# Kernel tuning notes

Measured on AMD Instinct MI355X. Metric: run time of the kernel, lower is better.

Reference implementation:

```python
import jax, jax.numpy as jnp
import numpy as np

N = 20000      # nodes
E = 320000     # edges (avg degree 16)
F_IN = 512     # post_features
H1, H2 = 1024, 512   # hard-coded GCN hidden widths
F_OUT = 128    # post_embedding
D1, D2 = 152, 48     # hard-coded Dense widths


def setup_inputs() -> dict:
    key = jax.random.key(0)
    ks = jax.random.split(key, 16)
    inp = {
        "x": jax.random.normal(ks[0], (N, F_IN), dtype=jnp.float32),
        "src": jax.random.randint(ks[1], (E,), 0, N, dtype=jnp.int32),
        "dst": jax.random.randint(ks[2], (E,), 0, N, dtype=jnp.int32),
        "edge_weight": jax.random.uniform(ks[3], (E,), dtype=jnp.float32) / 16.0,
        # GCN layer params (xavier-ish scale)
        "W1": jax.random.normal(ks[4], (F_IN, H1), dtype=jnp.float32) * (2.0 / (F_IN + H1)) ** 0.5,
        "b1": jax.random.uniform(ks[5], (H1,), dtype=jnp.float32),
        "W2": jax.random.normal(ks[6], (H1, H2), dtype=jnp.float32) * (2.0 / (H1 + H2)) ** 0.5,
        "b2": jax.random.uniform(ks[7], (H2,), dtype=jnp.float32),
        "W3": jax.random.normal(ks[8], (H2, F_OUT), dtype=jnp.float32) * (2.0 / (H2 + F_OUT)) ** 0.5,
        "b3": jax.random.uniform(ks[9], (F_OUT,), dtype=jnp.float32),
        # Dense head params
        "Wd1": jax.random.normal(ks[10], (F_OUT, D1), dtype=jnp.float32) * (2.0 / F_OUT) ** 0.5,
        "bd1": jnp.zeros((D1,), dtype=jnp.float32),
        "Wd2": jax.random.normal(ks[11], (D1, D2), dtype=jnp.float32) * (2.0 / D1) ** 0.5,
        "bd2": jnp.zeros((D2,), dtype=jnp.float32),
        "Wd3": jax.random.normal(ks[12], (D2, 1), dtype=jnp.float32) * (2.0 / D2) ** 0.5,
        "bd3": jnp.zeros((1,), dtype=jnp.float32),
    }
    return inp


def _spmm(src, dst, w, h, n):
    # out[i] = sum_{e: dst[e]==i} w[e] * h[src[e]]  == A @ h with A sparse COO
    return jax.ops.segment_sum(w[:, None] * h[src], dst, num_segments=n)


def reference(x, src, dst, edge_weight, W1, b1, W2, b2, W3, b3,
              Wd1, bd1, Wd2, bd2, Wd3, bd3):
    n = x.shape[0]
    # GCN layer: x @ W -> spmm(A, .) -> + bias ; tanh between layers 1,2
    h = jnp.tanh(_spmm(src, dst, edge_weight, x @ W1, n) + b1)
    h = jnp.tanh(_spmm(src, dst, edge_weight, h @ W2, n) + b2)
    g = _spmm(src, dst, edge_weight, h @ W3, n) + b3
    # F.dropout treated as identity (deterministic reference / eval mode)
    d = jax.nn.relu(g @ Wd1 + bd1)
    d = jax.nn.relu(d @ Wd2 + bd2)
    d = d @ Wd3 + bd3
    return d
```

## Files before the change

### kernel.cpp

```cpp
#include <hip/hip_runtime.h>
#include <hip/hip_bf16.h>


typedef __attribute__((ext_vector_type(8))) short bf16x8;
typedef __attribute__((ext_vector_type(8))) unsigned short u16x8;
typedef __attribute__((ext_vector_type(4))) float f32x4;
typedef unsigned short u16;

#define MPAD 20096
#define AS1 __attribute__((address_space(1)))
#define AS3 __attribute__((address_space(3)))

__device__ inline u16 f2b(float f) {
  union { float f; unsigned int u; } x; x.f = f;
  unsigned int r = x.u + 0x7FFFu + ((x.u >> 16) & 1u);
  return (u16)(r >> 16);
}
__device__ inline float b2f(u16 u) {
  union { unsigned int u; float f; } x; x.u = ((unsigned int)u) << 16; return x.f;
}
__device__ inline unsigned int cvt_pk_bf16(float lo, float hi) {
  unsigned int r;
  asm("v_cvt_pk_bf16_f32 %0, %1, %2" : "=v"(r) : "v"(lo), "v"(hi));
  return r;
}
__device__ inline float fast_tanh(float x) {
  float cx = fminf(fmaxf(x, -9.f), 9.f);
  float e = __expf(2.f * cx);
  float d = e + 1.f, r;
  asm("v_rcp_f32 %0, %1" : "=v"(r) : "v"(d));
  return (e - 1.f) * r;
}


__device__ inline void wT_tile(const float* __restrict__ W, u16* __restrict__ WT,
                               int K, int N, int KPAD, int NPAD,
                               int bx, int by, float (*tile)[33]) {
  const int kb = by * 32, nb = bx * 32;
  const int tx = threadIdx.x & 31, ty = threadIdx.x >> 5;
  #pragma unroll
  for (int i = 0; i < 4; ++i) {
    int k = kb + ty + i * 8, n = nb + tx;
    tile[ty + i * 8][tx] = (k < K && n < N) ? W[(size_t)k * N + n] : 0.f;
  }
  __syncthreads();
  #pragma unroll
  for (int i = 0; i < 4; ++i) {
    int n = nb + ty + i * 8, k = kb + tx;
    WT[(size_t)n * KPAD + k] = f2b(tile[tx][ty + i * 8]);
  }
}

__global__ __launch_bounds__(256) void prep_all(
    const float* __restrict__ x, u16* __restrict__ xb,
    const float* __restrict__ W1, u16* __restrict__ w1t,
    const float* __restrict__ W2, u16* __restrict__ w2t,
    const float* __restrict__ W3, u16* __restrict__ w3t,
    const float* __restrict__ Wd1, u16* __restrict__ wd1t,
    const float* __restrict__ Wd2, u16* __restrict__ wd2t,
    const float* __restrict__ bd1, float* __restrict__ bd1p,
    const float* __restrict__ bd2, float* __restrict__ bd2p,
    const int* __restrict__ dst, int* __restrict__ cnt1,
    int* __restrict__ cnt2) {
  __shared__ float tile[32][33];
  const int b = blockIdx.x;
  const int tid = threadIdx.x;
  if (b < 512) {
    wT_tile(W1, w1t, 512, 1024, 512, 1024, b % 32, b / 32, tile);
  } else if (b < 1024) {
    int t = b - 512;  wT_tile(W2, w2t, 1024, 512, 1024, 512, t % 16, t / 16, tile);
  } else if (b < 1088) {
    int t = b - 1024; wT_tile(W3, w3t, 512, 128, 512, 128, t % 4, t / 4, tile);
  } else if (b < 1120) {
    int t = b - 1088; wT_tile(Wd1, wd1t, 128, 152, 128, 256, t % 8, t / 8, tile);
  } else if (b < 1152) {
    int t = b - 1120; wT_tile(Wd2, wd2t, 152, 48, 256, 128, t % 4, t / 4, tile);
  } else if (b < 11152) {
    int idx = ((b - 1152) * 256 + tid) * 4;
    if (idx < 20000 * 512) {
      float4 v = *reinterpret_cast<const float4*>(&x[idx]);
      uint2 o;
      o.x = cvt_pk_bf16(v.x, v.y);
      o.y = cvt_pk_bf16(v.z, v.w);
      *reinterpret_cast<uint2*>(&xb[idx]) = o;
    }
  } else if (b == 11152) {
    bd1p[tid] = (tid < 152) ? bd1[tid] : 0.f;
  } else if (b == 11153) {
    if (tid < 128) bd2p[tid] = (tid < 48) ? bd2[tid] : 0.f;
  } else if (b < 12404) {
    int e = (b - 11154) * 256 + tid;
    if (e < 320000) atomicAdd(&cnt1[dst[e]], 1);
  } else {
    int i = (b - 12404) * 256 + tid;
    if (i < 20000) cnt2[i] = 0;
  }
}

__global__ __launch_bounds__(1024) void scan_part(
    const int* __restrict__ in, int* __restrict__ out,
    int* __restrict__ bsum, int n) {
  __shared__ int wsum[16];
  const int lane = threadIdx.x & 63, wv = threadIdx.x >> 6;
  int i = blockIdx.x * 1024 + threadIdx.x;
  int v = (i < n) ? in[i] : 0;
  int s = v;
  #pragma unroll
  for (int off = 1; off < 64; off <<= 1) {
    int t = __shfl_up(s, off, 64);
    if (lane >= off) s += t;
  }
  if (lane == 63) wsum[wv] = s;
  __syncthreads();
  if (wv == 0 && lane < 16) {
    int t = wsum[lane];
    #pragma unroll
    for (int off = 1; off < 16; off <<= 1) {
      int u = __shfl_up(t, off, 64);
      if (lane >= off) t += u;
    }
    wsum[lane] = t;
  }
  __syncthreads();
  int waveoff = (wv == 0) ? 0 : wsum[wv - 1];
  if (i < n) out[i] = waveoff + s - v;
  if (threadIdx.x == 0) bsum[blockIdx.x] = wsum[15];
}
__global__ __launch_bounds__(1024) void scan_fix(
    int* __restrict__ out, const int* __restrict__ bsum, int n, int nb) {
  int b = blockIdx.x;
  int pre = 0, tot = 0;
  for (int j = 0; j < nb; ++j) {
    int v = bsum[j];
    if (j < b) pre += v;
    tot += v;
  }
  int i = b * 1024 + threadIdx.x;
  if (i < n && b > 0) out[i] += pre;
  if (b == 0 && threadIdx.x == 0) out[n] = tot;
}

__global__ __launch_bounds__(256) void scatter_csr(
    const int* __restrict__ dst, const int* __restrict__ src,
    const float* __restrict__ ew, const int* __restrict__ row_ptr,
    int* __restrict__ cnt, int* __restrict__ csr_src,
    float* __restrict__ csr_w, int E) {
  int e = blockIdx.x * 256 + threadIdx.x;
  if (e >= E) return;
  int d = dst[e];
  int pos = row_ptr[d] + atomicAdd(&cnt[d], 1);
  csr_src[pos] = src[e];
  csr_w[pos] = ew[e];
}

template <int ACT, bool BIAS, bool OUT_BF16>
__global__ __launch_bounds__(256) void gemm_mfma_db(
    const u16* __restrict__ A, const u16* __restrict__ BT,
    const float* __restrict__ bias, void* __restrict__ C,
    int M, int K, int Nn) {
  __shared__ __align__(16) u16 As[2][128 * 64];
  __shared__ __align__(16) u16 Bs[2][128 * 64];
  const int tid = threadIdx.x;
  const int lane = tid & 63;
  const int wave = tid >> 6;
  const int lo = lane & 15, hi = lane >> 4;
  const int wr = wave >> 1, wc = wave & 1;

  const int gx = gridDim.x;
  const int nwg = gx * gridDim.y;
  const int wg = blockIdx.y * gx + blockIdx.x;
  const int q = nwg >> 3, r = nwg & 7;
  const int xcd = wg & 7, sidx = wg >> 3;
  const int swz = (xcd < r ? xcd * (q + 1) : r * (q + 1) + (xcd - r) * q) + sidx;
  const int row0 = (swz / gx) * 128;
  const int col0 = (swz % gx) * 128;

  const u16* pa[4];
  const u16* pb[4];
  int so[4];
  #pragma unroll
  for (int i = 0; i < 4; ++i) {
    int o = i * 4096 + tid * 16;
    int rr = o >> 7;
    int ke = ((o & 127) >> 1) ^ ((rr & 7) << 3);
    pa[i] = &A[(size_t)(row0 + rr) * K + ke];
    pb[i] = &BT[(size_t)(col0 + rr) * K + ke];
    so[i] = o >> 1;
  }

  const int nk = K >> 6;
  f32x4 acc[4][4] = {};

  auto STAGE = [&](int buf, int kt) {
    const int ko = kt << 6;
    #pragma unroll
    for (int i = 0; i < 4; ++i) {
      __builtin_amdgcn_global_load_lds(
          (const AS1 void*)(pa[i] + ko),
          (AS3 void*)&As[buf][so[i]], 16, 0, 0);
      __builtin_amdgcn_global_load_lds(
          (const AS1 void*)(pb[i] + ko),
          (AS3 void*)&Bs[buf][so[i]], 16, 0, 0);
    }
  };

  STAGE(0, 0);
  STAGE(1, 1);
  asm volatile("s_waitcnt vmcnt(8)" ::: "memory");
  __builtin_amdgcn_s_barrier();

  auto body = [&](int cur, int kt) {
    bf16x8 af[2][4], bfr[2][4];
    #pragma unroll
    for (int ks = 0; ks < 2; ++ks) {
      #pragma unroll
      for (int m = 0; m < 4; ++m) {
        int row = wr * 64 + m * 16 + lo;
        int idx = (row * 64 + ks * 32 + hi * 8) ^ ((row & 7) << 3);
        af[ks][m] = *reinterpret_cast<const bf16x8*>(&As[cur][idx]);
      }
      #pragma unroll
      for (int n = 0; n < 4; ++n) {
        int col = wc * 64 + n * 16 + lo;
        int idx = (col * 64 + ks * 32 + hi * 8) ^ ((col & 7) << 3);
        bfr[ks][n] = *reinterpret_cast<const bf16x8*>(&Bs[cur][idx]);
      }
    }
    __builtin_amdgcn_s_setprio(1);
    #pragma unroll
    for (int ks = 0; ks < 2; ++ks)
      #pragma unroll
      for (int m = 0; m < 4; ++m)
        #pragma unroll
        for (int n = 0; n < 4; ++n)
          acc[m][n] = __builtin_amdgcn_mfma_f32_16x16x32_bf16(
              af[ks][m], bfr[ks][n], acc[m][n], 0, 0, 0);
    __builtin_amdgcn_s_setprio(0);
    asm volatile("s_waitcnt lgkmcnt(0)" ::: "memory");
    __builtin_amdgcn_s_barrier();
    if (kt + 2 < nk) {
      STAGE(cur, kt + 2);
      asm volatile("s_waitcnt vmcnt(8)" ::: "memory");
    } else if (kt + 1 < nk) {
      asm volatile("s_waitcnt vmcnt(0)" ::: "memory");
    }
    __builtin_amdgcn_s_barrier();
  };

  for (int kt = 0; kt < nk; kt += 2) {
    body(0, kt);
    body(1, kt + 1);
  }

  float bv[4];
  if (BIAS) {
    #pragma unroll
    for (int n = 0; n < 4; ++n) bv[n] = bias[col0 + wc * 64 + n * 16 + lo];
  }

  u16* Cb = (u16*)C;
  float* Cf = (float*)C;
  #pragma unroll
  for (int m = 0; m < 4; ++m) {
    int rbase = row0 + wr * 64 + m * 16 + hi * 4;
    #pragma unroll
    for (int n = 0; n < 4; ++n) {
      int c = col0 + wc * 64 + n * 16 + lo;
      float vv[4];
      #pragma unroll
      for (int i = 0; i < 4; ++i) {
        float v = acc[m][n][i];
        if (BIAS) v += bv[n];
        if (ACT == 1) v = fast_tanh(v);
        else if (ACT == 2) v = fmaxf(v, 0.f);
        vv[i] = v;
      }
      if (OUT_BF16) {
        unsigned int r01 = cvt_pk_bf16(vv[0], vv[1]);
        unsigned int r23 = cvt_pk_bf16(vv[2], vv[3]);
        u16* p = Cb + (size_t)rbase * Nn + c;
        p[0]              = (u16)r01;
        p[Nn]             = (u16)(r01 >> 16);
        p[2 * (size_t)Nn] = (u16)r23;
        p[3 * (size_t)Nn] = (u16)(r23 >> 16);
      } else {
        float* p = Cf + (size_t)rbase * Nn + c;
        p[0] = vv[0]; p[Nn] = vv[1];
        p[2 * (size_t)Nn] = vv[2]; p[3 * (size_t)Nn] = vv[3];
      }
    }
  }
}

template <int ACT, bool BIAS, bool OUT_BF16>
__global__ __launch_bounds__(256) void spmm_wave512(
    const int* __restrict__ row_ptr, const int* __restrict__ csr_src,
    const float* __restrict__ csr_w, const u16* __restrict__ H,
    const float* __restrict__ bias, void* __restrict__ out, int N) {
  __shared__ int s_src[4][64];
  __shared__ float s_w[4][64];
  const int wv = threadIdx.x >> 6;
  const int lane = threadIdx.x & 63;
  const int node = blockIdx.x * 4 + wv;
  if (node >= N) return;
  const int c = lane * 8;
  const int beg = row_ptr[node], end = row_ptr[node + 1];

  float a[8] = {};
  for (int p = beg; p < end; p += 64) {
    int cnt = end - p;
    if (cnt > 64) cnt = 64;
    if (lane < cnt) {
      s_src[wv][lane] = csr_src[p + lane];
      s_w[wv][lane] = csr_w[p + lane];
    }
    asm volatile("s_waitcnt lgkmcnt(0)" ::: "memory");
    int j = 0;
    for (; j + 7 < cnt; j += 8) {
      int ss[8]; float ww[8]; u16x8 hh[8];
      #pragma unroll
      for (int u = 0; u < 8; ++u) { ss[u] = s_src[wv][j + u]; ww[u] = s_w[wv][j + u]; }
      #pragma unroll
      for (int u = 0; u < 8; ++u)
        hh[u] = *reinterpret_cast<const u16x8*>(&H[(size_t)ss[u] * 512 + c]);
      #pragma unroll
      for (int u = 0; u < 8; ++u)
        #pragma unroll
        for (int k = 0; k < 8; ++k) a[k] += ww[u] * b2f(hh[u][k]);
    }
    for (; j < cnt; ++j) {
      int s = s_src[wv][j];
      float wt = s_w[wv][j];
      u16x8 hv = *reinterpret_cast<const u16x8*>(&H[(size_t)s * 512 + c]);
      #pragma unroll
      for (int k = 0; k < 8; ++k) a[k] += wt * b2f(hv[k]);
    }
    asm volatile("s_waitcnt lgkmcnt(0)" ::: "memory");
  }
  if (BIAS) {
    #pragma unroll
    for (int k = 0; k < 8; ++k) a[k] += bias[c + k];
  }
  if (ACT == 1) {
    #pragma unroll
    for (int k = 0; k < 8; ++k) a[k] = fast_tanh(a[k]);
  }
  if (OUT_BF16) {
    uint4 o;
    o.x = cvt_pk_bf16(a[0], a[1]);
    o.y = cvt_pk_bf16(a[2], a[3]);
    o.z = cvt_pk_bf16(a[4], a[5]);
    o.w = cvt_pk_bf16(a[6], a[7]);
    *reinterpret_cast<uint4*>(&((u16*)out)[(size_t)node * 512 + c]) = o;
  } else {
    float* op = &((float*)out)[(size_t)node * 512 + c];
    #pragma unroll
    for (int k = 0; k < 8; ++k) op[k] = a[k];
  }
}

template <int F, int ACT, bool BIAS, bool OUT_BF16>
__global__ __launch_bounds__(256) void spmm_small(
    const int* __restrict__ row_ptr, const int* __restrict__ csr_src,
    const float* __restrict__ csr_w, const u16* __restrict__ H,
    const float* __restrict__ bias, void* __restrict__ out, int N) {
  constexpr int TPN = F / 8;
  constexpr int NPB = 256 / TPN;
  int sub = threadIdx.x / TPN;
  int ln = threadIdx.x - sub * TPN;
  int node = blockIdx.x * NPB + sub;
  if (node >= N) return;
  int c = ln * 8;
  int beg = row_ptr[node], end = row_ptr[node + 1];
  float a[8] = {};
  int p = beg;
  for (; p + 3 < end; p += 4) {
    int s0 = csr_src[p], s1 = csr_src[p + 1], s2 = csr_src[p + 2], s3 = csr_src[p + 3];
    float w0 = csr_w[p], w1 = csr_w[p + 1], w2 = csr_w[p + 2], w3 = csr_w[p + 3];
    u16x8 h0 = *reinterpret_cast<const u16x8*>(&H[(size_t)s0 * F + c]);
    u16x8 h1 = *reinterpret_cast<const u16x8*>(&H[(size_t)s1 * F + c]);
    u16x8 h2 = *reinterpret_cast<const u16x8*>(&H[(size_t)s2 * F + c]);
    u16x8 h3 = *reinterpret_cast<const u16x8*>(&H[(size_t)s3 * F + c]);
    #pragma unroll
    for (int k = 0; k < 8; ++k)
      a[k] += w0 * b2f(h0[k]) + w1 * b2f(h1[k]) +
              w2 * b2f(h2[k]) + w3 * b2f(h3[k]);
  }
  for (; p < end; ++p) {
    int s = csr_src[p];
    float wt = csr_w[p];
    u16x8 hv = *reinterpret_cast<const u16x8*>(&H[(size_t)s * F + c]);
    #pragma unroll
    for (int k = 0; k < 8; ++k) a[k] += wt * b2f(hv[k]);
  }
  if (BIAS) {
    #pragma unroll
    for (int k = 0; k < 8; ++k) a[k] += bias[c + k];
  }
  if (ACT == 1) {
    #pragma unroll
    for (int k = 0; k < 8; ++k) a[k] = fast_tanh(a[k]);
  }
  if (OUT_BF16) {
    uint4 o;
    o.x = cvt_pk_bf16(a[0], a[1]);
    o.y = cvt_pk_bf16(a[2], a[3]);
    o.z = cvt_pk_bf16(a[4], a[5]);
    o.w = cvt_pk_bf16(a[6], a[7]);
    *reinterpret_cast<uint4*>(&((u16*)out)[(size_t)node * F + c]) = o;
  } else {
    float* op = &((float*)out)[(size_t)node * F + c];
    #pragma unroll
    for (int k = 0; k < 8; ++k) op[k] = a[k];
  }
}

__global__ __launch_bounds__(256) void last_layer_bf16(
    const u16* __restrict__ D2v, const float* __restrict__ W,
    const float* __restrict__ b, float* __restrict__ out,
    int M, int K, int ld) {
  int rr = blockIdx.x * 256 + threadIdx.x;
  if (rr >= M) return;
  float s = b[0];
  const u16* row = &D2v[(size_t)rr * ld];
  #pragma unroll 8
  for (int k = 0; k < 48; ++k) s += b2f(row[k]) * W[k];
  out[rr] = s;
}


extern "C" void kernel_launch(void* const* d_in, const int* in_sizes, int n_in,
                              void* d_out, int out_size, void* d_ws, size_t ws_size,
                              hipStream_t stream) {
  const int N = 20000, E = 320000;
  const int F_IN = 512, H1 = 1024, H2 = 512, F_OUT = 128;
  const int D1P = 256, D2P = 128;

  const float* x    = (const float*)d_in[0];
  const int*   src  = (const int*)d_in[1];
  const int*   dst  = (const int*)d_in[2];
  const float* ew   = (const float*)d_in[3];
  const float* W1   = (const float*)d_in[4];
  const float* b1   = (const float*)d_in[5];
  const float* W2   = (const float*)d_in[6];
  const float* b2   = (const float*)d_in[7];
  const float* W3   = (const float*)d_in[8];
  const float* b3   = (const float*)d_in[9];
  const float* Wd1  = (const float*)d_in[10];
  const float* bd1  = (const float*)d_in[11];
  const float* Wd2  = (const float*)d_in[12];
  const float* bd2  = (const float*)d_in[13];
  const float* Wd3  = (const float*)d_in[14];
  const float* bd3  = (const float*)d_in[15];
  float* out = (float*)d_out;

  size_t off = 0;
  auto alloc = [&](size_t bytes) {
    void* p = (char*)d_ws + off;
    off += (bytes + 255) & ~(size_t)255;
    return p;
  };
  u16* xb   = (u16*)alloc((size_t)MPAD * F_IN * 2);
  u16* ax   = (u16*)alloc((size_t)MPAD * F_IN * 2);
  u16* h1   = (u16*)alloc((size_t)MPAD * H1 * 2);
  u16* w1t  = (u16*)alloc((size_t)H1 * F_IN * 2);
  u16* w2t  = (u16*)alloc((size_t)H2 * H1 * 2);
  u16* w3t  = (u16*)alloc((size_t)F_OUT * H2 * 2);
  u16* wd1t = (u16*)alloc((size_t)D1P * F_OUT * 2);
  u16* wd2t = (u16*)alloc((size_t)D2P * D1P * 2);
  float* bd1p = (float*)alloc((size_t)D1P * 4);
  float* bd2p = (float*)alloc((size_t)D2P * 4);
  int* row_ptr = (int*)alloc((size_t)(N + 1) * 4);
  int* cnt1    = (int*)alloc((size_t)N * 4);
  int* cnt2    = (int*)alloc((size_t)N * 4);
  int* bsum    = (int*)alloc((size_t)32 * 4);
  int* csr_src = (int*)alloc((size_t)E * 4);
  float* csr_w = (float*)alloc((size_t)E * 4);

  u16* t2 = xb;
  u16* h2 = ax;
  u16* t3 = h1;
  u16* gb = t3 + (size_t)MPAD * F_OUT;
  u16* d1 = gb + (size_t)MPAD * F_OUT;
  u16* d2 = d1 + (size_t)MPAD * D1P;

  auto cdiv = [](int a, int b) { return (a + b - 1) / b; };

  hipMemsetAsync(cnt1, 0, (size_t)N * 4, stream);
  prep_all<<<12483, 256, 0, stream>>>(x, xb, W1, w1t, W2, w2t, W3, w3t,
                                      Wd1, wd1t, Wd2, wd2t, bd1, bd1p,
                                      bd2, bd2p, dst, cnt1, cnt2);
  scan_part<<<20, 1024, 0, stream>>>(cnt1, row_ptr, bsum, N);
  scan_fix<<<20, 1024, 0, stream>>>(row_ptr, bsum, N, 20);
  scatter_csr<<<cdiv(E, 256), 256, 0, stream>>>(dst, src, ew, row_ptr, cnt2,
                                                csr_src, csr_w, E);

  spmm_wave512<0, false, true><<<cdiv(N, 4), 256, 0, stream>>>(
      row_ptr, csr_src, csr_w, xb, nullptr, ax, N);
  gemm_mfma_db<1, true, true><<<dim3(H1 / 128, MPAD / 128), 256, 0, stream>>>(
      ax, w1t, b1, h1, MPAD, F_IN, H1);

  gemm_mfma_db<0, false, true><<<dim3(H2 / 128, MPAD / 128), 256, 0, stream>>>(
      h1, w2t, nullptr, t2, MPAD, H1, H2);
  spmm_wave512<1, true, true><<<cdiv(N, 4), 256, 0, stream>>>(
      row_ptr, csr_src, csr_w, t2, b2, h2, N);

  gemm_mfma_db<0, false, true><<<dim3(F_OUT / 128, MPAD / 128), 256, 0, stream>>>(
      h2, w3t, nullptr, t3, MPAD, H2, F_OUT);
  spmm_small<128, 0, true, true><<<cdiv(N, 16), 256, 0, stream>>>(
      row_ptr, csr_src, csr_w, t3, b3, gb, N);

  gemm_mfma_db<2, true, true><<<dim3(D1P / 128, MPAD / 128), 256, 0, stream>>>(
      gb, wd1t, bd1p, d1, MPAD, F_OUT, D1P);
  gemm_mfma_db<2, true, true><<<dim3(D2P / 128, MPAD / 128), 256, 0, stream>>>(
      d1, wd2t, bd2p, d2, MPAD, D1P, D2P);
  last_layer_bf16<<<cdiv(N, 256), 256, 0, stream>>>(d2, Wd3, bd3, out, N, 48, D2P);
}
```

Measured before the change: 252.0 us.

## Pack CSR src/weight into u32 and split SpMM columns into per-XCD chunks

Packs each edge's source index (16 bits) and bf16-rounded weight into one 32-bit word, which halves CSR index traffic. The SpMM kernels are replaced by one kernel that splits the feature columns into chunks, with consecutive block IDs handling the same nodes' different column chunks. The intent is that the chunks land on different XCDs, so each XCD's L2 holds only a slice of H and cache locality improves. It depends on N < 65536 and on round-robin XCD dispatch, and it rounds edge weights to bf16, which costs some precision.

```diff
diff --git a/kernel.cpp b/kernel.cpp
--- a/kernel.cpp
+++ b/kernel.cpp
@@ -143,14 +143,12 @@
 __global__ __launch_bounds__(256) void scatter_csr(
     const int* __restrict__ dst, const int* __restrict__ src,
     const float* __restrict__ ew, const int* __restrict__ row_ptr,
-    int* __restrict__ cnt, int* __restrict__ csr_src,
-    float* __restrict__ csr_w, int E) {
+    int* __restrict__ cnt, unsigned int* __restrict__ csr_pack, int E) {
   int e = blockIdx.x * 256 + threadIdx.x;
   if (e >= E) return;
   int d = dst[e];
   int pos = row_ptr[d] + atomicAdd(&cnt[d], 1);
-  csr_src[pos] = src[e];
-  csr_w[pos] = ew[e];
+  csr_pack[pos] = ((unsigned int)f2b(ew[e]) << 16) | (unsigned int)src[e];
 }
 
 template <int ACT, bool BIAS, bool OUT_BF16>
@@ -292,126 +290,57 @@
   }
 }
 
-template <int ACT, bool BIAS, bool OUT_BF16>
-__global__ __launch_bounds__(256) void spmm_wave512(
-    const int* __restrict__ row_ptr, const int* __restrict__ csr_src,
-    const float* __restrict__ csr_w, const u16* __restrict__ H,
-    const float* __restrict__ bias, void* __restrict__ out, int N) {
-  __shared__ int s_src[4][64];
-  __shared__ float s_w[4][64];
-  const int wv = threadIdx.x >> 6;
-  const int lane = threadIdx.x & 63;
-  const int node = blockIdx.x * 4 + wv;
+template <int F, int CHUNKS, int ACT, bool BIAS, bool OUT_BF16>
+__global__ __launch_bounds__(256) void spmm_xcd(
+    const int* __restrict__ row_ptr, const unsigned int* __restrict__ pack,
+    const u16* __restrict__ H, const float* __restrict__ bias,
+    void* __restrict__ out, int N) {
+  const int ci = blockIdx.x % CHUNKS;
+  const int nb = blockIdx.x / CHUNKS;
+  const int g = threadIdx.x >> 4;
+  const int gl = threadIdx.x & 15;
+  const int node = nb * 16 + g;
   if (node >= N) return;
-  const int c = lane * 8;
+  const int c0 = ci * (F / CHUNKS) + gl * 4;
   const int beg = row_ptr[node], end = row_ptr[node + 1];
 
-  float a[8] = {};
-  for (int p = beg; p < end; p += 64) {
-    int cnt = end - p;
-    if (cnt > 64) cnt = 64;
-    if (lane < cnt) {
-      s_src[wv][lane] = csr_src[p + lane];
-      s_w[wv][lane] = csr_w[p + lane];
-    }
-    asm volatile("s_waitcnt lgkmcnt(0)" ::: "memory");
-    int j = 0;
-    for (; j + 7 < cnt; j += 8) {
-      int ss[8]; float ww[8]; u16x8 hh[8];
-      #pragma unroll
-      for (int u = 0; u < 8; ++u) { ss[u] = s_src[wv][j + u]; ww[u] = s_w[wv][j + u]; }
-      #pragma unroll
-      for (int u = 0; u < 8; ++u)
-        hh[u] = *reinterpret_cast<const u16x8*>(&H[(size_t)ss[u] * 512 + c]);
-      #pragma unroll
-      for (int u = 0; u < 8; ++u)
-        #pragma unroll
-        for (int k = 0; k < 8; ++k) a[k] += ww[u] * b2f(hh[u][k]);
-    }
-    for (; j < cnt; ++j) {
-      int s = s_src[wv][j];
-      float wt = s_w[wv][j];
-      u16x8 hv = *reinterpret_cast<const u16x8*>(&H[(size_t)s * 512 + c]);
-      #pragma unroll
-      for (int k = 0; k < 8; ++k) a[k] += wt * b2f(hv[k]);
-    }
-    asm volatile("s_waitcnt lgkmcnt(0)" ::: "memory");
-  }
-  if (BIAS) {
-    #pragma unroll
-    for (int k = 0; k < 8; ++k) a[k] += bias[c + k];
-  }
-  if (ACT == 1) {
-    #pragma unroll
-    for (int k = 0; k < 8; ++k) a[k] = fast_tanh(a[k]);
-  }
-  if (OUT_BF16) {
-    uint4 o;
-    o.x = cvt_pk_bf16(a[0], a[1]);
-    o.y = cvt_pk_bf16(a[2], a[3]);
-    o.z = cvt_pk_bf16(a[4], a[5]);
-    o.w = cvt_pk_bf16(a[6], a[7]);
-    *reinterpret_cast<uint4*>(&((u16*)out)[(size_t)node * 512 + c]) = o;
-  } else {
-    float* op = &((float*)out)[(size_t)node * 512 + c];
-    #pragma unroll
-    for (int k = 0; k < 8; ++k) op[k] = a[k];
-  }
-}
-
-template <int F, int ACT, bool BIAS, bool OUT_BF16>
-__global__ __launch_bounds__(256) void spmm_small(
-    const int* __restrict__ row_ptr, const int* __restrict__ csr_src,
-    const float* __restrict__ csr_w, const u16* __restrict__ H,
-    const float* __restrict__ bias, void* __restrict__ out, int N) {
-  constexpr int TPN = F / 8;
-  constexpr int NPB = 256 / TPN;
-  int sub = threadIdx.x / TPN;
-  int ln = threadIdx.x - sub * TPN;
-  int node = blockIdx.x * NPB + sub;
-  if (node >= N) return;
-  int c = ln * 8;
-  int beg = row_ptr[node], end = row_ptr[node + 1];
-  float a[8] = {};
+  float a0 = 0.f, a1 = 0.f, a2 = 0.f, a3 = 0.f;
   int p = beg;
   for (; p + 3 < end; p += 4) {
-    int s0 = csr_src[p], s1 = csr_src[p + 1], s2 = csr_src[p + 2], s3 = csr_src[p + 3];
-    float w0 = csr_w[p], w1 = csr_w[p + 1], w2 = csr_w[p + 2], w3 = csr_w[p + 3];
-    u16x8 h0 = *reinterpret_cast<const u16x8*>(&H[(size_t)s0 * F + c]);
-    u16x8 h1 = *reinterpret_cast<const u16x8*>(&H[(size_t)s1 * F + c]);
-    u16x8 h2 = *reinterpret_cast<const u16x8*>(&H[(size_t)s2 * F + c]);
-    u16x8 h3 = *reinterpret_cast<const u16x8*>(&H[(size_t)s3 * F + c]);
-    #pragma unroll
-    for (int k = 0; k < 8; ++k)
-      a[k] += w0 * b2f(h0[k]) + w1 * b2f(h1[k]) +
-              w2 * b2f(h2[k]) + w3 * b2f(h3[k]);
+    unsigned int k0 = pack[p], k1 = pack[p + 1], k2 = pack[p + 2], k3 = pack[p + 3];
+    ushort4 h0 = *reinterpret_cast<const ushort4*>(&H[(size_t)(k0 & 0xFFFFu) * F + c0]);
+    ushort4 h1 = *reinterpret_cast<const ushort4*>(&H[(size_t)(k1 & 0xFFFFu) * F + c0]);
+    ushort4 h2 = *reinterpret_cast<const ushort4*>(&H[(size_t)(k2 & 0xFFFFu) * F + c0]);
+    ushort4 h3 = *reinterpret_cast<const ushort4*>(&H[(size_t)(k3 & 0xFFFFu) * F + c0]);
+    float w0 = b2f((u16)(k0 >> 16)), w1 = b2f((u16)(k1 >> 16));
+    float w2 = b2f((u16)(k2 >> 16)), w3 = b2f((u16)(k3 >> 16));
+    a0 += w0 * b2f(h0.x) + w1 * b2f(h1.x) + w2 * b2f(h2.x) + w3 * b2f(h3.x);
+    a1 += w0 * b2f(h0.y) + w1 * b2f(h1.y) + w2 * b2f(h2.y) + w3 * b2f(h3.y);
+    a2 += w0 * b2f(h0.z) + w1 * b2f(h1.z) + w2 * b2f(h2.z) + w3 * b2f(h3.z);
+    a3 += w0 * b2f(h0.w) + w1 * b2f(h1.w) + w2 * b2f(h2.w) + w3 * b2f(h3.w);
   }
   for (; p < end; ++p) {
-    int s = csr_src[p];
-    float wt = csr_w[p];
-    u16x8 hv = *reinterpret_cast<const u16x8*>(&H[(size_t)s * F + c]);
-    #pragma unroll
-    for (int k = 0; k < 8; ++k) a[k] += wt * b2f(hv[k]);
+    unsigned int k0 = pack[p];
+    ushort4 h0 = *reinterpret_cast<const ushort4*>(&H[(size_t)(k0 & 0xFFFFu) * F + c0]);
+    float w0 = b2f((u16)(k0 >> 16));
+    a0 += w0 * b2f(h0.x); a1 += w0 * b2f(h0.y);
+    a2 += w0 * b2f(h0.z); a3 += w0 * b2f(h0.w);
   }
   if (BIAS) {
-    #pragma unroll
-    for (int k = 0; k < 8; ++k) a[k] += bias[c + k];
+    a0 += bias[c0]; a1 += bias[c0 + 1]; a2 += bias[c0 + 2]; a3 += bias[c0 + 3];
   }
   if (ACT == 1) {
-    #pragma unroll
-    for (int k = 0; k < 8; ++k) a[k] = fast_tanh(a[k]);
+    a0 = fast_tanh(a0); a1 = fast_tanh(a1);
+    a2 = fast_tanh(a2); a3 = fast_tanh(a3);
   }
   if (OUT_BF16) {
-    uint4 o;
-    o.x = cvt_pk_bf16(a[0], a[1]);
-    o.y = cvt_pk_bf16(a[2], a[3]);
-    o.z = cvt_pk_bf16(a[4], a[5]);
-    o.w = cvt_pk_bf16(a[6], a[7]);
-    *reinterpret_cast<uint4*>(&((u16*)out)[(size_t)node * F + c]) = o;
+    uint2 o;
+    o.x = cvt_pk_bf16(a0, a1);
+    o.y = cvt_pk_bf16(a2, a3);
+    *reinterpret_cast<uint2*>(&((u16*)out)[(size_t)node * F + c0]) = o;
   } else {
-    float* op = &((float*)out)[(size_t)node * F + c];
-    #pragma unroll
-    for (int k = 0; k < 8; ++k) op[k] = a[k];
+    float4 o = make_float4(a0, a1, a2, a3);
+    *reinterpret_cast<float4*>(&((float*)out)[(size_t)node * F + c0]) = o;
   }
 }
 
@@ -474,8 +403,7 @@
   int* cnt1    = (int*)alloc((size_t)N * 4);
   int* cnt2    = (int*)alloc((size_t)N * 4);
   int* bsum    = (int*)alloc((size_t)32 * 4);
-  int* csr_src = (int*)alloc((size_t)E * 4);
-  float* csr_w = (float*)alloc((size_t)E * 4);
+  unsigned int* csr_pack = (unsigned int*)alloc((size_t)E * 4);
 
   u16* t2 = xb;
   u16* h2 = ax;
@@ -485,6 +413,7 @@
   u16* d2 = d1 + (size_t)MPAD * D1P;
 
   auto cdiv = [](int a, int b) { return (a + b - 1) / b; };
+  const int NB16 = cdiv(N, 16);
 
   hipMemsetAsync(cnt1, 0, (size_t)N * 4, stream);
   prep_all<<<12483, 256, 0, stream>>>(x, xb, W1, w1t, W2, w2t, W3, w3t,
@@ -493,22 +422,22 @@
   scan_part<<<20, 1024, 0, stream>>>(cnt1, row_ptr, bsum, N);
   scan_fix<<<20, 1024, 0, stream>>>(row_ptr, bsum, N, 20);
   scatter_csr<<<cdiv(E, 256), 256, 0, stream>>>(dst, src, ew, row_ptr, cnt2,
-                                                csr_src, csr_w, E);
-
-  spmm_wave512<0, false, true><<<cdiv(N, 4), 256, 0, stream>>>(
-      row_ptr, csr_src, csr_w, xb, nullptr, ax, N);
+                                                csr_pack, E);
+
+  spmm_xcd<512, 8, 0, false, true><<<NB16 * 8, 256, 0, stream>>>(
+      row_ptr, csr_pack, xb, nullptr, ax, N);
   gemm_mfma_db<1, true, true><<<dim3(H1 / 128, MPAD / 128), 256, 0, stream>>>(
       ax, w1t, b1, h1, MPAD, F_IN, H1);
 
   gemm_mfma_db<0, false, true><<<dim3(H2 / 128, MPAD / 128), 256, 0, stream>>>(
       h1, w2t, nullptr, t2, MPAD, H1, H2);
-  spmm_wave512<1, true, true><<<cdiv(N, 4), 256, 0, stream>>>(
-      row_ptr, csr_src, csr_w, t2, b2, h2, N);
+  spmm_xcd<512, 8, 1, true, true><<<NB16 * 8, 256, 0, stream>>>(
+      row_ptr, csr_pack, t2, b2, h2, N);
 
   gemm_mfma_db<0, false, true><<<dim3(F_OUT / 128, MPAD / 128), 256, 0, stream>>>(
       h2, w3t, nullptr, t3, MPAD, H2, F_OUT);
-  spmm_small<128, 0, true, true><<<cdiv(N, 16), 256, 0, stream>>>(
-      row_ptr, csr_src, csr_w, t3, b3, gb, N);
+  spmm_xcd<128, 2, 0, true, true><<<NB16 * 2, 256, 0, stream>>>(
+      row_ptr, csr_pack, t3, b3, gb, N);
 
   gemm_mfma_db<2, true, true><<<dim3(D1P / 128, MPAD / 128), 256, 0, stream>>>(
       gb, wd1t, bd1p, d1, MPAD, F_OUT, D1P);
```

Result: faster. 245.3 us (-2.7%).
